# Performance work log

Hardware: AMD Instinct MI355X
Metric: run time of the kernel (lower is better)

Reference implementation:

```python
import jax, jax.numpy as jnp
import numpy as np

B, C, H, W = 1024, 3, 32, 32
NCLS = 10

def _conv(x, w, b, padding):
    y = jax.lax.conv_general_dilated(x, w, (1, 1), padding, dimension_numbers=('NCHW', 'OIHW', 'NCHW'))
    return y + b[None, :, None, None]

def _maxpool2(x):
    return jax.lax.reduce_window(x, -jnp.inf, jax.lax.max, (1, 1, 2, 2), (1, 1, 2, 2), 'VALID')

def _lenet(x, lw1, lb1, lw2, lb2, lfc1, lfb1, lfc2, lfb2, lfc3, lfb3):
    h = jax.nn.relu(_conv(x, lw1, lb1, 'VALID'))   # [B,6,28,28]
    h = _maxpool2(h)                               # [B,6,14,14]
    h = jax.nn.relu(_conv(h, lw2, lb2, 'VALID'))   # [B,16,10,10]
    h = _maxpool2(h)                               # [B,16,5,5]
    h = h.reshape(h.shape[0], -1)                  # [B,400]
    h = jax.nn.relu(h @ lfc1 + lfb1)
    h = jax.nn.relu(h @ lfc2 + lfb2)
    return h @ lfc3 + lfb3                         # [B,10]

def _resnet(x, rw0, rb0, rw1a, rb1a, rw1b, rb1b, rw2a, rb2a, rw2b, rb2b, rfc, rfb):
    h = jax.nn.relu(_conv(x, rw0, rb0, 'SAME'))    # [B,64,32,32]
    r = jax.nn.relu(_conv(h, rw1a, rb1a, 'SAME'))
    r = _conv(r, rw1b, rb1b, 'SAME')
    h = jax.nn.relu(h + r)
    r = jax.nn.relu(_conv(h, rw2a, rb2a, 'SAME'))
    r = _conv(r, rw2b, rb2b, 'SAME')
    h = jax.nn.relu(h + r)
    h = h.mean(axis=(2, 3))                        # [B,64]
    return h @ rfc + rfb                           # [B,10]

def setup_inputs():
    key = jax.random.key(0)
    ks = jax.random.split(key, 16)
    def w(k, shape, fan_in):
        return jax.random.normal(k, shape, jnp.float32) * np.float32(1.0 / np.sqrt(fan_in))
    return {
        'x': jax.random.normal(ks[0], (B, C, H, W), jnp.float32),
        'threshold': jnp.float32(0.3),
        'labels': jax.random.randint(ks[1], (B,), 0, NCLS),
        'lw1': w(ks[2], (6, 3, 5, 5), 75), 'lb1': jnp.zeros((6,), jnp.float32),
        'lw2': w(ks[3], (16, 6, 5, 5), 150), 'lb2': jnp.zeros((16,), jnp.float32),
        'lfc1': w(ks[4], (400, 120), 400), 'lfb1': jnp.zeros((120,), jnp.float32),
        'lfc2': w(ks[5], (120, 84), 120), 'lfb2': jnp.zeros((84,), jnp.float32),
        'lfc3': w(ks[6], (84, NCLS), 84), 'lfb3': jnp.zeros((NCLS,), jnp.float32),
        'rw0': w(ks[7], (64, 3, 3, 3), 27), 'rb0': jnp.zeros((64,), jnp.float32),
        'rw1a': w(ks[8], (64, 64, 3, 3), 576), 'rb1a': jnp.zeros((64,), jnp.float32),
        'rw1b': w(ks[9], (64, 64, 3, 3), 576), 'rb1b': jnp.zeros((64,), jnp.float32),
        'rw2a': w(ks[10], (64, 64, 3, 3), 576), 'rb2a': jnp.zeros((64,), jnp.float32),
        'rw2b': w(ks[11], (64, 64, 3, 3), 576), 'rb2b': jnp.zeros((64,), jnp.float32),
        'rfc': w(ks[12], (64, NCLS), 64), 'rfb': jnp.zeros((NCLS,), jnp.float32),
    }

def reference(x, threshold, labels, lw1, lb1, lw2, lb2, lfc1, lfb1, lfc2, lfb2, lfc3, lfb3, rw0, rb0, rw1a, rb1a, rw1b, rb1b, rw2a, rb2a, rw2b, rb2b, rfc, rfb):
    out = _lenet(x, lw1, lb1, lw2, lb2, lfc1, lfb1, lfc2, lfb2, lfc3, lfb3)
    pred = jnp.argmax(out, axis=1)
    # fused confusion-matrix update: single scatter-add replaces the 10x10 python loop
    conf_matrix = jnp.zeros((NCLS, NCLS), jnp.float32).at[labels, pred].add(1.0)
    probs = jax.nn.softmax(out, axis=1)
    top2, _ = jax.lax.top_k(probs, 2)
    low_conf = (top2[:, 0] - top2[:, 1]) <= threshold    # [B] bool
    # batched fallback: one grouped resnet call + masked merge replaces the per-sample loop
    res_out = _resnet(x, rw0, rb0, rw1a, rb1a, rw1b, rb1b, rw2a, rb2a, rw2b, rb2b, rfc, rfb)
    out = jnp.where(low_conf[:, None], res_out, out)
    return out, conf_matrix
```

## Files before the change

### kernel.cpp

```cpp
#include <hip/hip_runtime.h>
#include <hip/hip_bf16.h>
#include <math.h>

#define BATCH 1024

typedef __attribute__((ext_vector_type(8))) short bf16x8;
typedef __attribute__((ext_vector_type(4))) float f32x4;

#define IMG_ELEMS 73984
#define IMG_B 147968
#define ROW_B 4352
#define CH_B 544
#define WT_OFF 43520
#define WT_HALF_B 36864

__global__ __launch_bounds__(256) void lenet_conv1(const float* __restrict__ x,
    const float* __restrict__ w, const float* __restrict__ bias, float* __restrict__ p1)
{
    __shared__ float img[3 * 1024];
    __shared__ float wl[450];
    __shared__ float bl[6];
    int b = blockIdx.x, t = threadIdx.x;
    for (int i = t; i < 3072; i += 256) img[i] = x[(size_t)b * 3072 + i];
    for (int i = t; i < 450; i += 256) wl[i] = w[i];
    if (t < 6) bl[t] = bias[t];
    __syncthreads();
    for (int idx = t; idx < 1176; idx += 256) {
        int o = idx / 196, r = idx - o * 196, py = r / 14, px = r - py * 14;
        int y0 = 2 * py, x0 = 2 * px;
        float s00, s01, s10, s11;
        s00 = s01 = s10 = s11 = bl[o];
        for (int c = 0; c < 3; c++) {
            float pv[6][6];
            #pragma unroll
            for (int i2 = 0; i2 < 6; i2++)
                #pragma unroll
                for (int j2 = 0; j2 < 6; j2++)
                    pv[i2][j2] = img[c * 1024 + (y0 + i2) * 32 + x0 + j2];
            const float* wc = &wl[o * 75 + c * 25];
            #pragma unroll
            for (int ky = 0; ky < 5; ky++)
                #pragma unroll
                for (int kx = 0; kx < 5; kx++) {
                    float wv = wc[ky * 5 + kx];
                    s00 += pv[ky][kx] * wv;
                    s01 += pv[ky][kx + 1] * wv;
                    s10 += pv[ky + 1][kx] * wv;
                    s11 += pv[ky + 1][kx + 1] * wv;
                }
        }
        float m = fmaxf(fmaxf(s00, s01), fmaxf(s10, s11));
        p1[(size_t)b * 1176 + idx] = fmaxf(m, 0.f);
    }
}

__global__ __launch_bounds__(256) void lenet_conv2(const float* __restrict__ p1,
    const float* __restrict__ w, const float* __restrict__ bias, float* __restrict__ p2)
{
    __shared__ float img[1176];
    __shared__ float wl[2400];
    __shared__ float bl[16];
    int b = blockIdx.x, t = threadIdx.x;
    for (int i = t; i < 1176; i += 256) img[i] = p1[(size_t)b * 1176 + i];
    for (int i = t; i < 2400; i += 256) wl[i] = w[i];
    if (t < 16) bl[t] = bias[t];
    __syncthreads();
    for (int idx = t; idx < 400; idx += 256) {
        int o = idx / 25, r = idx - o * 25, py = r / 5, px = r - py * 5;
        int y0 = 2 * py, x0 = 2 * px;
        float s00, s01, s10, s11;
        s00 = s01 = s10 = s11 = bl[o];
        for (int c = 0; c < 6; c++) {
            float pv[6][6];
            #pragma unroll
            for (int i2 = 0; i2 < 6; i2++)
                #pragma unroll
                for (int j2 = 0; j2 < 6; j2++)
                    pv[i2][j2] = img[c * 196 + (y0 + i2) * 14 + x0 + j2];
            const float* wc = &wl[o * 150 + c * 25];
            #pragma unroll
            for (int ky = 0; ky < 5; ky++)
                #pragma unroll
                for (int kx = 0; kx < 5; kx++) {
                    float wv = wc[ky * 5 + kx];
                    s00 += pv[ky][kx] * wv;
                    s01 += pv[ky][kx + 1] * wv;
                    s10 += pv[ky + 1][kx] * wv;
                    s11 += pv[ky + 1][kx + 1] * wv;
                }
        }
        float m = fmaxf(fmaxf(s00, s01), fmaxf(s10, s11));
        p2[(size_t)b * 400 + idx] = fmaxf(m, 0.f);
    }
}

__global__ __launch_bounds__(256) void lenet_fc(const float* __restrict__ p2,
    const float* __restrict__ w1, const float* __restrict__ b1,
    const float* __restrict__ w2, const float* __restrict__ b2,
    const float* __restrict__ w3, const float* __restrict__ b3,
    const int* __restrict__ labels, const float* __restrict__ thr,
    float* __restrict__ out, float* __restrict__ conf, int* __restrict__ flags)
{
    __shared__ float xin[400];
    __shared__ float h1[120];
    __shared__ float h2[84];
    __shared__ float ps[256];
    __shared__ float lg[10];
    int b = blockIdx.x, t = threadIdx.x;
    for (int i = t; i < 400; i += 256) xin[i] = p2[(size_t)b * 400 + i];
    __syncthreads();
    {
        int n = t & 127, half = t >> 7;
        float s = 0.f;
        if (n < 120) {
            int k0 = half * 200;
            for (int k = k0; k < k0 + 200; k++) s += xin[k] * w1[k * 120 + n];
        }
        ps[t] = s;
    }
    __syncthreads();
    if (t < 120) h1[t] = fmaxf(ps[t] + ps[t + 128] + b1[t], 0.f);
    __syncthreads();
    {
        int n = t & 127, half = t >> 7;
        float s = 0.f;
        if (n < 84) {
            int k0 = half * 60;
            for (int k = k0; k < k0 + 60; k++) s += h1[k] * w2[k * 84 + n];
        }
        ps[t] = s;
    }
    __syncthreads();
    if (t < 84) h2[t] = fmaxf(ps[t] + ps[t + 128] + b2[t], 0.f);
    __syncthreads();
    if (t < 10) {
        float s = b3[t];
        for (int k = 0; k < 84; k++) s += h2[k] * w3[k * 10 + t];
        lg[t] = s;
        out[(size_t)b * 10 + t] = s;
    }
    __syncthreads();
    if (t == 0) {
        int pred = 0;
        float m = lg[0];
        #pragma unroll
        for (int j = 1; j < 10; j++) if (lg[j] > m) { m = lg[j]; pred = j; }
        float se = 0.f, m2 = -1e30f;
        #pragma unroll
        for (int j = 0; j < 10; j++) {
            se += expf(lg[j] - m);
            if (j != pred) m2 = fmaxf(m2, lg[j]);
        }
        float gap = (1.f - expf(m2 - m)) / se;
        flags[b] = (gap <= thr[0]) ? 1 : 0;
        atomicAdd(&conf[labels[b] * 10 + pred], 1.f);
    }
}

__global__ __launch_bounds__(256) void prep_weights(
    const float* __restrict__ w0, const float* __restrict__ w1,
    const float* __restrict__ w2, const float* __restrict__ w3,
    __hip_bfloat16* __restrict__ dst)
{
    int tid = blockIdx.x * 256 + threadIdx.x;
    if (tid >= 4 * 36864) return;
    int c = tid / 36864, r = tid - c * 36864;
    int tap = r / 4096, r2 = r - tap * 4096;
    int co = r2 >> 6, ci = r2 & 63;
    const float* src = (c == 0) ? w0 : (c == 1) ? w1 : (c == 2) ? w2 : w3;
    float v = src[((size_t)co * 64 + ci) * 9 + tap];
    int nh = co >> 5, nt = (co >> 4) & 1, m = co & 15;
    int kb = ci >> 5, q = (ci >> 3) & 3, e = ci & 7;
    size_t elem = (size_t)(c * 2 + nh) * 18432
                + (size_t)((tap * 2 + kb) * 2 + nt) * 512 + q * 128 + m * 8 + e;
    dst[elem] = __float2bfloat16(v);
}

__global__ __launch_bounds__(256) void prep_w0t(const float* __restrict__ w,
                                                float* __restrict__ dst)
{
    int tid = blockIdx.x * 256 + threadIdx.x;
    if (tid >= 1728) return;
    int k = tid >> 6, co = tid & 63;
    dst[tid] = w[co * 27 + k];
}

__global__ __launch_bounds__(256) void zero_borders(__hip_bfloat16* __restrict__ buf, int cb)
{
    int tid = blockIdx.x * 256 + threadIdx.x;
    int total = cb * 132 * 8;
    if (tid >= total) return;
    int img = tid / 1056, r = tid - img * 1056;
    int pxi = r >> 3, chunk = r & 7;
    int row, col;
    if (pxi < 34)       { row = 0;  col = pxi; }
    else if (pxi < 68)  { row = 33; col = pxi - 34; }
    else if (pxi < 100) { row = pxi - 67; col = 0; }
    else                { row = pxi - 99; col = 33; }
    uint4 z = {0, 0, 0, 0};
    *(uint4*)((char*)buf + (size_t)img * IMG_B + (size_t)row * ROW_B
              + chunk * CH_B + col * 16) = z;
}

__global__ __launch_bounds__(256) void conv0_nhwc(const float* __restrict__ x,
    const float* __restrict__ wT, const float* __restrict__ bias,
    __hip_bfloat16* __restrict__ out, int cb)
{
    __shared__ char smem[8 * ROW_B];
    float* sl = (float*)smem;
    int bid = blockIdx.x;
    int img = bid % cb, strip = bid / cb;
    int r0 = strip * 8;
    int t = threadIdx.x;
    const float* xi = x + (size_t)img * 3072;
    for (int i = t; i < 1020; i += 256) {
        int c = i / 340, rr2 = i - c * 340;
        int rr = rr2 / 34, cc = rr2 - rr * 34;
        int y = r0 + rr - 1, xx = cc - 1;
        float v = 0.f;
        if (y >= 0 && y < 32 && xx >= 0 && xx < 32) v = xi[c * 1024 + y * 32 + xx];
        sl[(c * 10 + rr) * 34 + cc] = v;
    }
    __syncthreads();

    int rr = t >> 5, col = t & 31;
    float iv[27];
    #pragma unroll
    for (int c = 0; c < 3; c++)
        #pragma unroll
        for (int dy = 0; dy < 3; dy++)
            #pragma unroll
            for (int dx = 0; dx < 3; dx++)
                iv[c * 9 + dy * 3 + dx] = sl[(c * 10 + rr + dy) * 34 + col + dx];
    __syncthreads();

    float s[64];
    #pragma unroll
    for (int co = 0; co < 64; co++) s[co] = bias[co];
    #pragma unroll
    for (int k = 0; k < 27; k++) {
        const float v = iv[k];
        const float* wk = wT + k * 64;
        #pragma unroll
        for (int co = 0; co < 64; co++) s[co] = fmaf(v, wk[co], s[co]);
    }
    __hip_bfloat16 ov[64];
    #pragma unroll
    for (int co = 0; co < 64; co++) ov[co] = __float2bfloat16(fmaxf(s[co], 0.f));

    char* brow = smem + rr * ROW_B + (col + 1) * 16;
    const uint4* srcv = (const uint4*)ov;
    #pragma unroll
    for (int j = 0; j < 8; j++) *(uint4*)(brow + j * CH_B) = srcv[j];
    if (t < 128) {
        int row = t >> 4, ch = (t >> 1) & 7, side = t & 1;
        uint4 z = {0, 0, 0, 0};
        *(uint4*)(smem + row * ROW_B + ch * CH_B + (side ? 33 : 0) * 16) = z;
    }
    __syncthreads();
    char* gbase = (char*)out + (size_t)img * IMG_B + (size_t)(r0 + 1) * ROW_B;
    for (int u = t; u < 2176; u += 256)
        *(uint4*)(gbase + (size_t)u * 16) = *(const uint4*)(smem + (size_t)u * 16);
}

#define GLL(gp, lp)                                                            \
    __builtin_amdgcn_global_load_lds(                                          \
        (const __attribute__((address_space(1))) unsigned int*)(gp),           \
        (__attribute__((address_space(3))) unsigned int*)(lp), 16, 0, 0)

template<bool ADD>
__global__ __launch_bounds__(256, 2) void conv3x3_lds(
    const __hip_bfloat16* __restrict__ act, const __hip_bfloat16* __restrict__ wts,
    const float* __restrict__ bias, const __hip_bfloat16* __restrict__ skip,
    __hip_bfloat16* __restrict__ out, int cb)
{
    __shared__ char sl[WT_OFF + WT_HALF_B];
    int bid = blockIdx.x;
    int task = (bid & 7) * (gridDim.x >> 3) + (bid >> 3);
    int img = task >> 3;
    int rem = task & 7;
    int strip = rem >> 1, nh = rem & 1;
    int t = threadIdx.x;
    int w = t >> 6, lane = t & 63;
    int m = lane & 15, q = lane >> 4;

    const char* gsrc = (const char*)act + (size_t)img * IMG_B + (size_t)(strip * 8) * ROW_B;
    for (int u0 = w * 64; u0 < 2720; u0 += 256) {
        int u = u0 + lane;
        if (u < 2720)
            GLL(gsrc + (size_t)u * 16, sl + u0 * 16);
    }
    const char* gw = (const char*)wts + (size_t)nh * WT_HALF_B;
    for (int u0 = w * 64; u0 < 2304; u0 += 256)
        GLL(gw + (size_t)(u0 + lane) * 16, sl + WT_OFF + u0 * 16);
    __syncthreads();

    int xbase[4];
    #pragma unroll
    for (int nt = 0; nt < 4; nt++)
        xbase[nt] = (2 * w + (nt >> 1)) * ROW_B + ((nt & 1) * 16 + m) * 16 + q * CH_B;
    int wbase[2];
    #pragma unroll
    for (int mt = 0; mt < 2; mt++)
        wbase[mt] = WT_OFF + mt * 1024 + q * 256 + m * 16;

    f32x4 acc[2][4] = {};
    bf16x8 a[2][4], b[2][2];

    #define XLOAD(s, buf)                                                      \
        {                                                                      \
            const int tap_ = (s) >> 1, kb_ = (s) & 1;                          \
            const int off_ = (tap_ / 3) * ROW_B + (tap_ - (tap_ / 3) * 3) * 16 \
                           + kb_ * (4 * CH_B);                                 \
            _Pragma("unroll")                                                  \
            for (int nt = 0; nt < 4; nt++)                                     \
                a[buf][nt] = *(const bf16x8*)(sl + xbase[nt] + off_);          \
        }
    #define WLOAD(s, buf)                                                      \
        {                                                                      \
            const int off_ = ((s) >> 1) * 4096 + ((s) & 1) * 2048;             \
            _Pragma("unroll")                                                  \
            for (int mt = 0; mt < 2; mt++)                                     \
                b[buf][mt] = *(const bf16x8*)(sl + wbase[mt] + off_);          \
        }

    XLOAD(0, 0) WLOAD(0, 0)
    #pragma unroll
    for (int s = 0; s < 18; s++) {
        int cur = s & 1;
        if (s < 17) { XLOAD(s + 1, cur ^ 1) WLOAD(s + 1, cur ^ 1) }
        #pragma unroll
        for (int mt = 0; mt < 2; mt++)
            #pragma unroll
            for (int nt = 0; nt < 4; nt++)
                acc[mt][nt] = __builtin_amdgcn_mfma_f32_16x16x32_bf16(
                    b[cur][mt], a[cur][nt], acc[mt][nt], 0, 0, 0);
    }
    #undef XLOAD
    #undef WLOAD

    char* oimg = (char*)out + (size_t)img * IMG_B;
    const char* simg = (const char*)skip + (size_t)img * IMG_B;
    float4 bv4[2];
    #pragma unroll
    for (int mt = 0; mt < 2; mt++)
        bv4[mt] = *(const float4*)(bias + nh * 32 + mt * 16 + q * 4);

    size_t goff[2][4];
    #pragma unroll
    for (int mt = 0; mt < 2; mt++)
        #pragma unroll
        for (int nt = 0; nt < 4; nt++)
            goff[mt][nt] = (size_t)(strip * 8 + 1 + 2 * w + (nt >> 1)) * ROW_B
                         + (nh * 4 + 2 * mt + (q >> 1)) * CH_B
                         + (m + (nt & 1) * 16 + 1) * 16 + (q & 1) * 8;

    union { uint2 u; __hip_bfloat16 h[4]; } sk[2][4];
    if (ADD) {
        #pragma unroll
        for (int mt = 0; mt < 2; mt++)
            #pragma unroll
            for (int nt = 0; nt < 4; nt++)
                sk[mt][nt].u = *(const uint2*)(simg + goff[mt][nt]);
    }
    #pragma unroll
    for (int mt = 0; mt < 2; mt++) {
        #pragma unroll
        for (int nt = 0; nt < 4; nt++) {
            union { uint2 u; __hip_bfloat16 h[4]; } pk;
            #pragma unroll
            for (int r = 0; r < 4; r++) {
                float f = acc[mt][nt][r] + ((const float*)&bv4[mt])[r];
                if (ADD) f += __bfloat162float(sk[mt][nt].h[r]);
                pk.h[r] = __float2bfloat16(fmaxf(f, 0.f));
            }
            *(uint2*)(oimg + goff[mt][nt]) = pk.u;
        }
    }
}

__global__ __launch_bounds__(256) void res_head_bf16(const __hip_bfloat16* __restrict__ h,
    const float* __restrict__ rfc, const float* __restrict__ rfb,
    const int* __restrict__ flags, float* __restrict__ out)
{
    __shared__ float part[4][64];
    __shared__ float mns[64];
    int img = blockIdx.x, t = threadIdx.x;
    int w = t >> 6, lane = t & 63;
    int c = lane & 7;
    const char* base = (const char*)h + (size_t)img * IMG_B;

    float s8[8];
    #pragma unroll
    for (int j = 0; j < 8; j++) s8[j] = 0.f;

    for (int ry = 0; ry < 8; ry++) {
        int row = w * 8 + ry + 1;
        const char* rb = base + (size_t)row * ROW_B;
        #pragma unroll
        for (int k = 0; k < 4; k++) {
            int g = lane + 64 * k;
            bf16x8 v = *(const bf16x8*)(rb + c * CH_B + ((g >> 3) + 1) * 16);
            #pragma unroll
            for (int j = 0; j < 8; j++)
                s8[j] += __bfloat162float(*(__hip_bfloat16*)&((short*)&v)[j]);
        }
    }
    #pragma unroll
    for (int off = 8; off <= 32; off <<= 1)
        #pragma unroll
        for (int j = 0; j < 8; j++) s8[j] += __shfl_xor(s8[j], off, 64);
    if (lane < 8)
        #pragma unroll
        for (int j = 0; j < 8; j++) part[w][c * 8 + j] = s8[j];
    __syncthreads();
    if (t < 64) mns[t] = (part[0][t] + part[1][t] + part[2][t] + part[3][t]) * (1.f / 1024.f);
    __syncthreads();
    if (t < 10 && flags[img]) {
        float s2 = rfb[t];
        for (int cc = 0; cc < 64; cc++) s2 += mns[cc] * rfc[cc * 10 + t];
        out[(size_t)img * 10 + t] = s2;
    }
}

extern "C" void kernel_launch(void* const* d_in, const int* in_sizes, int n_in,
                              void* d_out, int out_size, void* d_ws, size_t ws_size,
                              hipStream_t stream)
{
    const float* x    = (const float*)d_in[0];
    const float* thr  = (const float*)d_in[1];
    const int*   labels = (const int*)d_in[2];
    const float* lw1 = (const float*)d_in[3];  const float* lb1 = (const float*)d_in[4];
    const float* lw2 = (const float*)d_in[5];  const float* lb2 = (const float*)d_in[6];
    const float* lfc1 = (const float*)d_in[7]; const float* lfb1 = (const float*)d_in[8];
    const float* lfc2 = (const float*)d_in[9]; const float* lfb2 = (const float*)d_in[10];
    const float* lfc3 = (const float*)d_in[11];const float* lfb3 = (const float*)d_in[12];
    const float* rw0 = (const float*)d_in[13]; const float* rb0 = (const float*)d_in[14];
    const float* rw1a = (const float*)d_in[15];const float* rb1a = (const float*)d_in[16];
    const float* rw1b = (const float*)d_in[17];const float* rb1b = (const float*)d_in[18];
    const float* rw2a = (const float*)d_in[19];const float* rb2a = (const float*)d_in[20];
    const float* rw2b = (const float*)d_in[21];const float* rb2b = (const float*)d_in[22];
    const float* rfc = (const float*)d_in[23]; const float* rfb = (const float*)d_in[24];

    float* out  = (float*)d_out;
    float* conf = out + (size_t)BATCH * 10;

    int nc = 1;
    while (nc < 16 &&
           2ull * (size_t)(BATCH / nc) * 147968ull + 294912ull + 16384ull > ws_size)
        nc <<= 1;
    int cb = BATCH / nc;

    __hip_bfloat16* A  = (__hip_bfloat16*)d_ws;
    __hip_bfloat16* Bb = A + (size_t)cb * IMG_ELEMS;
    __hip_bfloat16* wprep = Bb + (size_t)cb * IMG_ELEMS;
    int* flags = (int*)((char*)wprep + 294912);
    float* w0t = (float*)((char*)wprep + 294912 + 4096);

    float* p1 = (float*)A;
    float* p2 = p1 + 1204224;

    hipMemsetAsync(conf, 0, 100 * sizeof(float), stream);

    prep_weights<<<(4 * 36864 + 255) / 256, 256, 0, stream>>>(rw1a, rw1b, rw2a, rw2b, wprep);
    prep_w0t<<<7, 256, 0, stream>>>(rw0, w0t);

    lenet_conv1<<<BATCH, 256, 0, stream>>>(x, lw1, lb1, p1);
    lenet_conv2<<<BATCH, 256, 0, stream>>>(p1, lw2, lb2, p2);
    lenet_fc<<<BATCH, 256, 0, stream>>>(p2, lfc1, lfb1, lfc2, lfb2, lfc3, lfb3,
                                        labels, thr, out, conf, flags);

    int zb = (cb * 1056 + 255) / 256;
    zero_borders<<<zb, 256, 0, stream>>>(A, cb);
    zero_borders<<<zb, 256, 0, stream>>>(Bb, cb);

    const __hip_bfloat16* W1a = wprep;
    const __hip_bfloat16* W1b = wprep + 36864;
    const __hip_bfloat16* W2a = wprep + 2 * 36864;
    const __hip_bfloat16* W2b = wprep + 3 * 36864;

    for (int c0 = 0; c0 < BATCH; c0 += cb) {
        const float* xc = x + (size_t)c0 * 3072;
        conv0_nhwc<<<cb * 4, 256, 0, stream>>>(xc, w0t, rb0, A, cb);
        conv3x3_lds<false><<<cb * 8, 256, 0, stream>>>(A,  W1a, rb1a, nullptr, Bb, cb);
        conv3x3_lds<true ><<<cb * 8, 256, 0, stream>>>(Bb, W1b, rb1b, A, A, cb);
        conv3x3_lds<false><<<cb * 8, 256, 0, stream>>>(A,  W2a, rb2a, nullptr, Bb, cb);
        conv3x3_lds<true ><<<cb * 8, 256, 0, stream>>>(Bb, W2b, rb2b, A, A, cb);
        res_head_bf16<<<cb, 256, 0, stream>>>(A, rfc, rfb, flags + c0, out + (size_t)c0 * 10);
    }
}
```

Before: 632.1 us.

## Enlarge conv3x3 tiles to half-image by all 64 output channels per block

Each conv3x3 block now covers 16 rows of an image and all 64 output channels using 512 threads, instead of 8 rows and 32 channels with 256 threads. Each wave computes four output-channel tiles, so every activation fragment loaded from LDS feeds twice as many MFMAs. Halo rows are also loaded far less redundantly across blocks. In exchange the kernel uses about 152KB of LDS and runs one block per CU with more accumulator registers, which cuts latency hiding and gives a quarter as many blocks.

```diff
diff --git a/kernel.cpp b/kernel.cpp
--- a/kernel.cpp
+++ b/kernel.cpp
@@ -11,8 +11,8 @@
 #define IMG_B 147968
 #define ROW_B 4352
 #define CH_B 544
-#define WT_OFF 43520
 #define WT_HALF_B 36864
+#define WT2_OFF 78336
 
 __global__ __launch_bounds__(256) void lenet_conv1(const float* __restrict__ x,
     const float* __restrict__ w, const float* __restrict__ bias, float* __restrict__ p1)
@@ -269,43 +269,40 @@
         (__attribute__((address_space(3))) unsigned int*)(lp), 16, 0, 0)
 
 template<bool ADD>
-__global__ __launch_bounds__(256, 2) void conv3x3_lds(
+__global__ __launch_bounds__(512, 1) void conv3x3_lds(
     const __hip_bfloat16* __restrict__ act, const __hip_bfloat16* __restrict__ wts,
     const float* __restrict__ bias, const __hip_bfloat16* __restrict__ skip,
     __hip_bfloat16* __restrict__ out, int cb)
 {
-    __shared__ char sl[WT_OFF + WT_HALF_B];
+    __shared__ char sl[152064];
     int bid = blockIdx.x;
     int task = (bid & 7) * (gridDim.x >> 3) + (bid >> 3);
-    int img = task >> 3;
-    int rem = task & 7;
-    int strip = rem >> 1, nh = rem & 1;
+    int img = task >> 1, h = task & 1;
     int t = threadIdx.x;
     int w = t >> 6, lane = t & 63;
     int m = lane & 15, q = lane >> 4;
 
-    const char* gsrc = (const char*)act + (size_t)img * IMG_B + (size_t)(strip * 8) * ROW_B;
-    for (int u0 = w * 64; u0 < 2720; u0 += 256) {
+    const char* gsrc = (const char*)act + (size_t)img * IMG_B + (size_t)(h * 16) * ROW_B;
+    for (int u0 = w * 64; u0 < 4896; u0 += 512) {
         int u = u0 + lane;
-        if (u < 2720)
-            GLL(gsrc + (size_t)u * 16, sl + u0 * 16);
-    }
-    const char* gw = (const char*)wts + (size_t)nh * WT_HALF_B;
-    for (int u0 = w * 64; u0 < 2304; u0 += 256)
-        GLL(gw + (size_t)(u0 + lane) * 16, sl + WT_OFF + u0 * 16);
+        if (u < 4896) GLL(gsrc + (size_t)u * 16, sl + u0 * 16);
+    }
+    const char* gw = (const char*)wts;
+    for (int u0 = w * 64; u0 < 4608; u0 += 512)
+        GLL(gw + (size_t)(u0 + lane) * 16, sl + WT2_OFF + u0 * 16);
     __syncthreads();
 
     int xbase[4];
     #pragma unroll
     for (int nt = 0; nt < 4; nt++)
         xbase[nt] = (2 * w + (nt >> 1)) * ROW_B + ((nt & 1) * 16 + m) * 16 + q * CH_B;
-    int wbase[2];
-    #pragma unroll
-    for (int mt = 0; mt < 2; mt++)
-        wbase[mt] = WT_OFF + mt * 1024 + q * 256 + m * 16;
-
-    f32x4 acc[2][4] = {};
-    bf16x8 a[2][4], b[2][2];
+    int wbase[4];
+    #pragma unroll
+    for (int mt = 0; mt < 4; mt++)
+        wbase[mt] = WT2_OFF + (mt >> 1) * WT_HALF_B + (mt & 1) * 1024 + q * 256 + m * 16;
+
+    f32x4 acc[4][4] = {};
+    bf16x8 a[2][4], b[2][4];
 
     #define XLOAD(s, buf)                                                      \
         {                                                                      \
@@ -320,7 +317,7 @@
         {                                                                      \
             const int off_ = ((s) >> 1) * 4096 + ((s) & 1) * 2048;             \
             _Pragma("unroll")                                                  \
-            for (int mt = 0; mt < 2; mt++)                                     \
+            for (int mt = 0; mt < 4; mt++)                                     \
                 b[buf][mt] = *(const bf16x8*)(sl + wbase[mt] + off_);          \
         }
 
@@ -330,7 +327,7 @@
         int cur = s & 1;
         if (s < 17) { XLOAD(s + 1, cur ^ 1) WLOAD(s + 1, cur ^ 1) }
         #pragma unroll
-        for (int mt = 0; mt < 2; mt++)
+        for (int mt = 0; mt < 4; mt++)
             #pragma unroll
             for (int nt = 0; nt < 4; nt++)
                 acc[mt][nt] = __builtin_amdgcn_mfma_f32_16x16x32_bf16(
@@ -341,40 +338,36 @@
 
     char* oimg = (char*)out + (size_t)img * IMG_B;
     const char* simg = (const char*)skip + (size_t)img * IMG_B;
-    float4 bv4[2];
-    #pragma unroll
-    for (int mt = 0; mt < 2; mt++)
-        bv4[mt] = *(const float4*)(bias + nh * 32 + mt * 16 + q * 4);
-
-    size_t goff[2][4];
-    #pragma unroll
-    for (int mt = 0; mt < 2; mt++)
-        #pragma unroll
-        for (int nt = 0; nt < 4; nt++)
-            goff[mt][nt] = (size_t)(strip * 8 + 1 + 2 * w + (nt >> 1)) * ROW_B
-                         + (nh * 4 + 2 * mt + (q >> 1)) * CH_B
-                         + (m + (nt & 1) * 16 + 1) * 16 + (q & 1) * 8;
-
-    union { uint2 u; __hip_bfloat16 h[4]; } sk[2][4];
-    if (ADD) {
-        #pragma unroll
-        for (int mt = 0; mt < 2; mt++)
-            #pragma unroll
-            for (int nt = 0; nt < 4; nt++)
-                sk[mt][nt].u = *(const uint2*)(simg + goff[mt][nt]);
-    }
-    #pragma unroll
-    for (int mt = 0; mt < 2; mt++) {
+    float4 bv4[4];
+    #pragma unroll
+    for (int mt = 0; mt < 4; mt++)
+        bv4[mt] = *(const float4*)(bias + (mt >> 1) * 32 + (mt & 1) * 16 + q * 4);
+
+    #pragma unroll
+    for (int mt = 0; mt < 4; mt++) {
         #pragma unroll
         for (int nt = 0; nt < 4; nt++) {
-            union { uint2 u; __hip_bfloat16 h[4]; } pk;
-            #pragma unroll
-            for (int r = 0; r < 4; r++) {
-                float f = acc[mt][nt][r] + ((const float*)&bv4[mt])[r];
-                if (ADD) f += __bfloat162float(sk[mt][nt].h[r]);
-                pk.h[r] = __float2bfloat16(fmaxf(f, 0.f));
+            size_t goff = (size_t)(h * 16 + 1 + 2 * w + (nt >> 1)) * ROW_B
+                        + ((mt >> 1) * 4 + (mt & 1) * 2 + (q >> 1)) * CH_B
+                        + (m + (nt & 1) * 16 + 1) * 16 + (q & 1) * 8;
+            union { uint2 u; __hip_bfloat16 h4[4]; } pk;
+            if (ADD) {
+                union { uint2 u; __hip_bfloat16 h4[4]; } sk;
+                sk.u = *(const uint2*)(simg + goff);
+                #pragma unroll
+                for (int r = 0; r < 4; r++) {
+                    float f = acc[mt][nt][r] + ((const float*)&bv4[mt])[r]
+                            + __bfloat162float(sk.h4[r]);
+                    pk.h4[r] = __float2bfloat16(fmaxf(f, 0.f));
+                }
+            } else {
+                #pragma unroll
+                for (int r = 0; r < 4; r++) {
+                    float f = acc[mt][nt][r] + ((const float*)&bv4[mt])[r];
+                    pk.h4[r] = __float2bfloat16(fmaxf(f, 0.f));
+                }
             }
-            *(uint2*)(oimg + goff[mt][nt]) = pk.u;
+            *(uint2*)(oimg + goff) = pk.u;
         }
     }
 }
@@ -482,10 +475,10 @@
     for (int c0 = 0; c0 < BATCH; c0 += cb) {
         const float* xc = x + (size_t)c0 * 3072;
         conv0_nhwc<<<cb * 4, 256, 0, stream>>>(xc, w0t, rb0, A, cb);
-        conv3x3_lds<false><<<cb * 8, 256, 0, stream>>>(A,  W1a, rb1a, nullptr, Bb, cb);
-        conv3x3_lds<true ><<<cb * 8, 256, 0, stream>>>(Bb, W1b, rb1b, A, A, cb);
-        conv3x3_lds<false><<<cb * 8, 256, 0, stream>>>(A,  W2a, rb2a, nullptr, Bb, cb);
-        conv3x3_lds<true ><<<cb * 8, 256, 0, stream>>>(Bb, W2b, rb2b, A, A, cb);
+        conv3x3_lds<false><<<cb * 2, 512, 0, stream>>>(A,  W1a, rb1a, nullptr, Bb, cb);
+        conv3x3_lds<true ><<<cb * 2, 512, 0, stream>>>(Bb, W1b, rb1b, A, A, cb);
+        conv3x3_lds<false><<<cb * 2, 512, 0, stream>>>(A,  W2a, rb2a, nullptr, Bb, cb);
+        conv3x3_lds<true ><<<cb * 2, 512, 0, stream>>>(Bb, W2b, rb2b, A, A, cb);
         res_head_bf16<<<cb, 256, 0, stream>>>(A, rfc, rfb, flags + c0, out + (size_t)c0 * 10);
     }
 }
```

Measured after the change: 670.7 us. 6.1% more time.
